# Kernel optimization log

Measured on AMD Instinct MI355X. Metric: run time of the kernel, lower is better.

Reference implementation:

```python
import jax, jax.numpy as jnp
import numpy as np

DIM = 1024
HEADS = 16
HEAD_DIM = DIM // HEADS
NEG = -1e30
EPS = 1e-5


def _linear(x, w, b):
    # torch nn.Linear: y = x @ W^T + b, W: [out, in]
    return jnp.einsum('bnd,od->bno', x, w) + b


def _mha(x, ctx, wq, bq, wk, bk, wv, bv, wo, bo, mask):
    B, N, D = x.shape
    M = ctx.shape[1]
    q = _linear(x, wq, bq).reshape(B, N, HEADS, HEAD_DIM).transpose(0, 2, 1, 3)
    k = _linear(ctx, wk, bk).reshape(B, M, HEADS, HEAD_DIM).transpose(0, 2, 1, 3)
    v = _linear(ctx, wv, bv).reshape(B, M, HEADS, HEAD_DIM).transpose(0, 2, 1, 3)
    scores = jnp.einsum('bhqd,bhkd->bhqk', q, k) / np.sqrt(HEAD_DIM).astype(np.float32)
    if mask is not None:
        scores = jnp.where(mask == 0, NEG, scores)
    attn = jax.nn.softmax(scores, axis=-1)  # dropout = identity (eval mode)
    out = jnp.einsum('bhqk,bhkd->bhqd', attn, v)
    out = out.transpose(0, 2, 1, 3).reshape(B, N, D)
    return _linear(out, wo, bo)


def _ln(x, g, b):
    mu = jnp.mean(x, axis=-1, keepdims=True)
    var = jnp.mean(jnp.square(x - mu), axis=-1, keepdims=True)
    return (x - mu) * jax.lax.rsqrt(var + EPS) * g + b


def setup_inputs() -> dict:
    key = jax.random.key(0)
    ks = jax.random.split(key, 24)
    B, N, M = 2, 2048, 1024
    s = 0.02
    d = {
        'x': jax.random.normal(ks[0], (B, N, DIM), jnp.float32),
        'memory': jax.random.normal(ks[1], (B, M, DIM), jnp.float32),
        'mask': jnp.tril(jnp.ones((N, N), jnp.int32))[None, None],
    }
    i = 2
    for p in ['sa', 'ca']:
        for nm in ['q', 'k', 'v', 'o']:
            d[f'{p}_w{nm}'] = jax.random.normal(ks[i], (DIM, DIM), jnp.float32) * s; i += 1
            d[f'{p}_b{nm}'] = jnp.zeros((DIM,), jnp.float32)
    d['ff_w1'] = jax.random.normal(ks[i], (4 * DIM, DIM), jnp.float32) * s; i += 1
    d['ff_b1'] = jnp.zeros((4 * DIM,), jnp.float32)
    d['ff_w2'] = jax.random.normal(ks[i], (DIM, 4 * DIM), jnp.float32) * s; i += 1
    d['ff_b2'] = jnp.zeros((DIM,), jnp.float32)
    for j in (1, 2, 3):
        d[f'ln{j}_g'] = jnp.ones((DIM,), jnp.float32)
        d[f'ln{j}_b'] = jnp.zeros((DIM,), jnp.float32)
    return d


def reference(x, memory, mask,
              sa_wq, sa_bq, sa_wk, sa_bk, sa_wv, sa_bv, sa_wo, sa_bo,
              ca_wq, ca_bq, ca_wk, ca_bk, ca_wv, ca_bv, ca_wo, ca_bo,
              ff_w1, ff_b1, ff_w2, ff_b2,
              ln1_g, ln1_b, ln2_g, ln2_b, ln3_g, ln3_b):
    x = _ln(x + _mha(x, x, sa_wq, sa_bq, sa_wk, sa_bk, sa_wv, sa_bv, sa_wo, sa_bo, mask), ln1_g, ln1_b)
    x = _ln(x + _mha(x, memory, ca_wq, ca_bq, ca_wk, ca_bk, ca_wv, ca_bv, ca_wo, ca_bo, None), ln2_g, ln2_b)
    h = jax.nn.relu(_linear(x, ff_w1, ff_b1))  # dropout = identity (eval)
    x = _ln(x + _linear(h, ff_w2, ff_b2), ln3_g, ln3_b)
    return x
```

## Files before the change

### kernel.cpp

```cpp
#include <hip/hip_runtime.h>


typedef __attribute__((ext_vector_type(8))) short bf16x8;
typedef __attribute__((ext_vector_type(4))) float f32x4;

__device__ __forceinline__ unsigned short f2bf(float f) {
    union { float f; unsigned int u; } v; v.f = f;
    unsigned int r = v.u + 0x7fffu + ((v.u >> 16) & 1u);
    return (unsigned short)(r >> 16);
}
__device__ __forceinline__ unsigned int bftrunc(float f) {
    union { float f; unsigned int u; } v; v.f = f;
    return v.u >> 16;
}

struct ConvArgs {
    const float* src[12];
    unsigned short* dst[12];
    int blk_ofs[13];
    int n4[12];
};
__global__ __launch_bounds__(256) void conv_multi(ConvArgs a)
{
    int bid = blockIdx.x;
    int s = 0;
#pragma unroll
    for (int t = 0; t < 12; ++t) if (bid >= a.blk_ofs[t + 1]) s = t + 1;
    int i = (bid - a.blk_ofs[s]) * 256 + threadIdx.x;
    if (i >= a.n4[s]) return;
    float4 v = ((const float4*)a.src[s])[i];
    ushort4 o;
    o.x = f2bf(v.x); o.y = f2bf(v.y); o.z = f2bf(v.z); o.w = f2bf(v.w);
    ((ushort4*)a.dst[s])[i] = o;
}

__global__ __launch_bounds__(256) void concat_bias(
    const float* __restrict__ bq, const float* __restrict__ bk,
    const float* __restrict__ bv, const float* __restrict__ ck,
    const float* __restrict__ cv, float* __restrict__ bqkv,
    float* __restrict__ bkvc)
{
    int i = blockIdx.x * 256 + threadIdx.x;
    if (i < 1024)       bqkv[i] = bq[i];
    else if (i < 2048)  bqkv[i] = bk[i - 1024];
    else if (i < 3072)  bqkv[i] = bv[i - 2048];
    else if (i < 4096)  bkvc[i - 3072] = ck[i - 3072];
    else if (i < 5120)  bkvc[i - 3072] = cv[i - 4096];
}

template<int TM, int TN, int EPI, int SK>
__global__ __launch_bounds__(256) void gemm_bt(
    const unsigned short* __restrict__ A, const unsigned short* __restrict__ W,
    const float* __restrict__ bias, void* __restrict__ out,
    int K, int Ncols, long slice_stride)
{
    constexpr int AI = TM / 32;
    constexpr int BJ = TN / 32;
    __shared__ unsigned short As[TM][64];
    __shared__ unsigned short Bs[TN][64];

    const int tid  = threadIdx.x;
    const int lane = tid & 63;
    const int wave = tid >> 6;
    const int qd   = lane >> 4;
    const int l15  = lane & 15;
    const int wm   = (wave >> 1) * (TM / 2);
    const int wn   = (wave & 1) * (TN / 2);

    const int gx  = gridDim.x;
    const int bid = blockIdx.y * gx + blockIdx.x;
    const int gpg = 8 * gx;
    const long m0 = (long)((bid / gpg) * 8 + (bid & 7)) * TM;
    const long n0 = (long)((bid % gpg) >> 3) * TN;

    f32x4 acc[AI][BJ] = {};

    const int srow = lane >> 3;
    const int scol = (((lane & 7) ^ srow)) * 8;
    const unsigned short* Ag = A + (m0 + wave * (8 * AI) + srow) * (long)K + scol;
    const unsigned short* Wg = W + (n0 + wave * (8 * BJ) + srow) * (long)K + scol;

    const int ksl   = K / SK;
    const int kbase = (SK > 1) ? (int)blockIdx.z * ksl : 0;

    for (int k0 = kbase; k0 < kbase + ksl; k0 += 64) {
#pragma unroll
        for (int c = 0; c < AI; ++c)
            __builtin_amdgcn_global_load_lds(
                (const __attribute__((address_space(1))) unsigned int*)(Ag + (long)c * 8 * K + k0),
                (__attribute__((address_space(3))) unsigned int*)((char*)&As[0][0] + (wave * AI + c) * 1024),
                16, 0, 0);
#pragma unroll
        for (int c = 0; c < BJ; ++c)
            __builtin_amdgcn_global_load_lds(
                (const __attribute__((address_space(1))) unsigned int*)(Wg + (long)c * 8 * K + k0),
                (__attribute__((address_space(3))) unsigned int*)((char*)&Bs[0][0] + (wave * BJ + c) * 1024),
                16, 0, 0);
        __syncthreads();
#pragma unroll
        for (int kk = 0; kk < 64; kk += 32) {
            const int pg = ((((kk >> 3) + qd)) ^ (l15 & 7)) * 8;
            bf16x8 af[AI], bw[BJ];
#pragma unroll
            for (int i = 0; i < AI; ++i)
                af[i] = *(const bf16x8*)&As[wm + i * 16 + l15][pg];
#pragma unroll
            for (int j = 0; j < BJ; ++j)
                bw[j] = *(const bf16x8*)&Bs[wn + j * 16 + l15][pg];
#pragma unroll
            for (int i = 0; i < AI; ++i)
#pragma unroll
                for (int j = 0; j < BJ; ++j)
                    acc[i][j] = __builtin_amdgcn_mfma_f32_16x16x32_bf16(
                        af[i], bw[j], acc[i][j], 0, 0, 0);
        }
        __syncthreads();
    }

    float* op = (float*)out + ((SK > 1) ? (long)blockIdx.z * slice_stride : 0);
#pragma unroll
    for (int j = 0; j < BJ; ++j) {
        long col = n0 + wn + j * 16 + l15;
        float bv = (SK == 1 || blockIdx.z == 0) ? bias[col] : 0.f;
#pragma unroll
        for (int i = 0; i < AI; ++i) {
#pragma unroll
            for (int r = 0; r < 4; ++r) {
                long row = m0 + wm + i * 16 + qd * 4 + r;
                float v = acc[i][j][r] + bv;
                if (EPI == 0) {
                    op[row * Ncols + col] = v;
                } else if (EPI == 1) {
                    ((unsigned short*)out)[row * Ncols + col] = f2bf(v);
                } else {
                    ((unsigned short*)out)[row * Ncols + col] = f2bf(v > 0.f ? v : 0.f);
                }
            }
        }
    }
}

__global__ __launch_bounds__(256) void attn_kernel(
    const unsigned short* __restrict__ Qb, int q_stride,
    const unsigned short* __restrict__ KVb, int kv_stride, int koff, int voff,
    unsigned short* __restrict__ O,
    int Nq, int Mk, int causal)
{
    __shared__ unsigned short Ks[64][72];
    __shared__ unsigned short Vs[64][72];
    __shared__ unsigned short Ps[4][16][72];

    const int tid  = threadIdx.x;
    const int lane = tid & 63;
    const int wave = tid >> 6;
    const int qd   = lane >> 4;
    const int l15  = lane & 15;
    const int h    = blockIdx.y;
    const int b    = blockIdx.z;
    int jq = blockIdx.x;
    if (causal && (b & 1)) jq = gridDim.x - 1 - jq;
    const int q0 = jq * 64;
    const int tb = q0 + wave * 16;

    bf16x8 aq0, aq1;
    {
        const unsigned short* qp =
            Qb + (long)(b * Nq + tb + l15) * q_stride + h * 64 + qd * 8;
        aq0 = *(const bf16x8*)qp;
        aq1 = *(const bf16x8*)(qp + 32);
    }

    float lpart[4] = {};
    f32x4 oacc[4] = {};

    const int krow = tid >> 3;
    const int kcol = (tid & 7) * 8;
    const int vj   = tid & 31;
    const int va_k = (vj & 15) + ((vj & 16) << 1);
    const int vfg  = (tid >> 5) * 8;
    const int vpc  = (va_k & 15) * 4 + (va_k >> 4);

    const unsigned short* Kg = KVb + (long)b * Mk * kv_stride + koff + h * 64;
    const unsigned short* Vg = KVb + (long)b * Mk * kv_stride + voff + h * 64;

    bf16x8 kr0, kr1, vra, vrb;
    auto prefetch = [&](int k0) {
        kr0 = *(const bf16x8*)(Kg + (long)(k0 + krow) * kv_stride + kcol);
        kr1 = *(const bf16x8*)(Kg + (long)(k0 + krow + 32) * kv_stride + kcol);
        const unsigned short* v0 = Vg + (long)(k0 + va_k) * kv_stride + vfg;
        vra = *(const bf16x8*)v0;
        vrb = *(const bf16x8*)(v0 + 16 * kv_stride);
    };

    const int nk = causal ? (q0 + 64) : Mk;
    prefetch(0);
    const float SCL = 0.125f * 1.44269504f;

    for (int k0 = 0; k0 < nk; k0 += 64) {
        __syncthreads();
        *(bf16x8*)&Ks[krow][kcol]      = kr0;
        *(bf16x8*)&Ks[krow + 32][kcol] = kr1;
#pragma unroll
        for (int jf = 0; jf < 8; ++jf) {
            unsigned int d = (unsigned short)vra[jf] |
                             ((unsigned int)(unsigned short)vrb[jf] << 16);
            *(unsigned int*)&Vs[vfg + jf][vpc] = d;
        }
        if (k0 + 64 < nk) prefetch(k0 + 64);
        __syncthreads();

        if (!causal || (k0 <= tb + 15)) {
            bf16x8 bk[4][2];
#pragma unroll
            for (int kt = 0; kt < 4; ++kt)
#pragma unroll
                for (int c = 0; c < 2; ++c)
                    bk[kt][c] = *(const bf16x8*)&Ks[kt * 16 + l15][c * 32 + qd * 8];
            f32x4 s[4];
#pragma unroll
            for (int kt = 0; kt < 4; ++kt) {
                f32x4 z = {};
                z = __builtin_amdgcn_mfma_f32_16x16x32_bf16(aq0, bk[kt][0], z, 0, 0, 0);
                z = __builtin_amdgcn_mfma_f32_16x16x32_bf16(aq1, bk[kt][1], z, 0, 0, 0);
                s[kt] = z;
            }
            const bool needmask = causal && (k0 + 63 > tb);
#pragma unroll
            for (int r = 0; r < 4; ++r) {
                const int qg = tb + qd * 4 + r;
                float e[4];
#pragma unroll
                for (int kt = 0; kt < 4; ++kt) {
                    float ev = __builtin_amdgcn_exp2f(s[kt][r] * SCL);
                    if (needmask && (k0 + kt * 16 + l15 > qg)) ev = 0.f;
                    e[kt] = ev;
                }
                lpart[r] += (e[0] + e[1]) + (e[2] + e[3]);
                unsigned int lo = bftrunc(e[0]) | (bftrunc(e[1]) << 16);
                unsigned int hi = bftrunc(e[2]) | (bftrunc(e[3]) << 16);
                uint2 pk; pk.x = lo; pk.y = hi;
                *(uint2*)&Ps[wave][qd * 4 + r][l15 * 4] = pk;
            }
            bf16x8 bv[4][2];
#pragma unroll
            for (int dt = 0; dt < 4; ++dt)
#pragma unroll
                for (int c = 0; c < 2; ++c)
                    bv[dt][c] = *(const bf16x8*)&Vs[dt * 16 + l15][c * 32 + qd * 8];
            bf16x8 ap0 = *(const bf16x8*)&Ps[wave][l15][qd * 8];
            bf16x8 ap1 = *(const bf16x8*)&Ps[wave][l15][32 + qd * 8];
#pragma unroll
            for (int dt = 0; dt < 4; ++dt) {
                oacc[dt] = __builtin_amdgcn_mfma_f32_16x16x32_bf16(
                    ap0, bv[dt][0], oacc[dt], 0, 0, 0);
                oacc[dt] = __builtin_amdgcn_mfma_f32_16x16x32_bf16(
                    ap1, bv[dt][1], oacc[dt], 0, 0, 0);
            }
        }
    }

#pragma unroll
    for (int r = 0; r < 4; ++r) {
        float l = lpart[r];
        l += __shfl_xor(l, 1);
        l += __shfl_xor(l, 2);
        l += __shfl_xor(l, 4);
        l += __shfl_xor(l, 8);
        float inv = 1.f / l;
        long row = (long)(b * Nq + tb + qd * 4 + r);
#pragma unroll
        for (int dt = 0; dt < 4; ++dt)
            O[row * 1024 + h * 64 + dt * 16 + l15] = f2bf(oacc[dt][r] * inv);
    }
}

template<int ND>
__global__ __launch_bounds__(256) void ln_res_kernel(
    const float* __restrict__ res, const float* __restrict__ delta, long dstride,
    const float* __restrict__ g, const float* __restrict__ beta,
    float* __restrict__ yout, unsigned short* __restrict__ ybf)
{
    __shared__ float red[8];
    const int row = blockIdx.x;
    const int tid = threadIdx.x;
    const long base = (long)row * 1024 + tid * 4;
    float4 a = *(const float4*)(res + base);
    float v0 = a.x, v1 = a.y, v2 = a.z, v3 = a.w;
#pragma unroll
    for (int t = 0; t < ND; ++t) {
        float4 d = *(const float4*)(delta + t * dstride + base);
        v0 += d.x; v1 += d.y; v2 += d.z; v3 += d.w;
    }
    float s  = v0 + v1 + v2 + v3;
    float ss = v0 * v0 + v1 * v1 + v2 * v2 + v3 * v3;
#pragma unroll
    for (int off = 1; off < 64; off <<= 1) {
        s  += __shfl_xor(s, off);
        ss += __shfl_xor(ss, off);
    }
    const int wave = tid >> 6;
    if ((tid & 63) == 0) { red[wave] = s; red[4 + wave] = ss; }
    __syncthreads();
    float st  = red[0] + red[1] + red[2] + red[3];
    float sst = red[4] + red[5] + red[6] + red[7];
    float mean = st * (1.f / 1024.f);
    float var  = sst * (1.f / 1024.f) - mean * mean;
    float inv  = rsqrtf(var + 1e-5f);
    const int c = tid * 4;
    float y0 = (v0 - mean) * inv * g[c + 0] + beta[c + 0];
    float y1 = (v1 - mean) * inv * g[c + 1] + beta[c + 1];
    float y2 = (v2 - mean) * inv * g[c + 2] + beta[c + 2];
    float y3 = (v3 - mean) * inv * g[c + 3] + beta[c + 3];
    *(float4*)(yout + base) = make_float4(y0, y1, y2, y3);
    if (ybf) {
        ushort4 o;
        o.x = f2bf(y0); o.y = f2bf(y1); o.z = f2bf(y2); o.w = f2bf(y3);
        *(ushort4*)(ybf + base) = o;
    }
}

extern "C" void kernel_launch(void* const* d_in, const int* in_sizes, int n_in,
                              void* d_out, int out_size, void* d_ws, size_t ws_size,
                              hipStream_t stream)
{
    const int B = 2, N = 2048, M = 1024, D = 1024, FF = 4096;
    const int TN = B * N;
    const int TM = B * M;
    const size_t MB = 1024 * 1024;

    const float* x     = (const float*)d_in[0];
    const float* mem   = (const float*)d_in[1];
    const float* sa_wq = (const float*)d_in[3];  const float* sa_bq = (const float*)d_in[4];
    const float* sa_wk = (const float*)d_in[5];  const float* sa_bk = (const float*)d_in[6];
    const float* sa_wv = (const float*)d_in[7];  const float* sa_bv = (const float*)d_in[8];
    const float* sa_wo = (const float*)d_in[9];  const float* sa_bo = (const float*)d_in[10];
    const float* ca_wq = (const float*)d_in[11]; const float* ca_bq = (const float*)d_in[12];
    const float* ca_wk = (const float*)d_in[13]; const float* ca_bk = (const float*)d_in[14];
    const float* ca_wv = (const float*)d_in[15]; const float* ca_bv = (const float*)d_in[16];
    const float* ca_wo = (const float*)d_in[17]; const float* ca_bo = (const float*)d_in[18];
    const float* ff_w1 = (const float*)d_in[19]; const float* ff_b1 = (const float*)d_in[20];
    const float* ff_w2 = (const float*)d_in[21]; const float* ff_b2 = (const float*)d_in[22];
    const float* ln1_g = (const float*)d_in[23]; const float* ln1_b = (const float*)d_in[24];
    const float* ln2_g = (const float*)d_in[25]; const float* ln2_b = (const float*)d_in[26];
    const float* ln3_g = (const float*)d_in[27]; const float* ln3_b = (const float*)d_in[28];

    char* w = (char*)d_ws;
    size_t off = 0;
    auto alloc = [&](size_t bytes) -> char* {
        char* p = w + off; off += (bytes + 255) & ~(size_t)255; return p;
    };

    unsigned short* xb   = (unsigned short*)alloc((size_t)TN * D * 2);
    unsigned short* memb = (unsigned short*)alloc((size_t)TM * D * 2);
    unsigned short* wqkv = (unsigned short*)alloc((size_t)3 * D * D * 2);
    unsigned short* wos  = (unsigned short*)alloc((size_t)D * D * 2);
    unsigned short* wqc  = (unsigned short*)alloc((size_t)D * D * 2);
    unsigned short* wkvc = (unsigned short*)alloc((size_t)2 * D * D * 2);
    unsigned short* woc  = (unsigned short*)alloc((size_t)D * D * 2);
    unsigned short* w1b  = (unsigned short*)alloc((size_t)FF * D * 2);
    unsigned short* w2b  = (unsigned short*)alloc((size_t)D * FF * 2);
    float* xf = (float*)alloc((size_t)TN * D * 4);
    char* big = alloc((size_t)64 * MB);
    unsigned short* qkv = (unsigned short*)big;
    unsigned short* kvb = (unsigned short*)big;
    unsigned short* qb  = (unsigned short*)(big + 8 * MB);
    unsigned short* ab  = (unsigned short*)(big + 24 * MB);
    unsigned short* hb  = (unsigned short*)big;
    float*          tmp = (float*)(big + 32 * MB);
    const long      TSL = (long)TN * D;
    float* bqkv = (float*)alloc((size_t)3 * D * 4);
    float* bkvc = (float*)alloc((size_t)2 * D * 4);

    ConvArgs ca;
    const float* srcs[12] = {x, mem, sa_wq, sa_wk, sa_wv, sa_wo,
                             ca_wq, ca_wk, ca_wv, ca_wo, ff_w1, ff_w2};
    unsigned short* dsts[12] = {xb, memb, wqkv, wqkv + (size_t)D * D,
                                wqkv + (size_t)2 * D * D, wos, wqc, wkvc,
                                wkvc + (size_t)D * D, woc, w1b, w2b};
    long ns[12] = {(long)TN * D, (long)TM * D, (long)D * D, (long)D * D,
                   (long)D * D, (long)D * D, (long)D * D, (long)D * D,
                   (long)D * D, (long)D * D, (long)FF * D, (long)D * FF};
    int total_blk = 0;
    for (int i = 0; i < 12; ++i) {
        ca.src[i] = srcs[i]; ca.dst[i] = dsts[i];
        ca.n4[i] = (int)(ns[i] / 4);
        ca.blk_ofs[i] = total_blk;
        total_blk += (ca.n4[i] + 255) / 256;
    }
    ca.blk_ofs[12] = total_blk;
    conv_multi<<<dim3(total_blk), dim3(256), 0, stream>>>(ca);
    concat_bias<<<dim3(20), dim3(256), 0, stream>>>(
        sa_bq, sa_bk, sa_bv, ca_bk, ca_bv, bqkv, bkvc);

    dim3 blk(256);

    gemm_bt<128, 128, 1, 1><<<dim3(3 * D / 128, TN / 128), blk, 0, stream>>>(
        xb, wqkv, bqkv, qkv, D, 3 * D, 0);
    attn_kernel<<<dim3(N / 64, 16, B), blk, 0, stream>>>(
        qkv, 3 * D, qkv, 3 * D, D, 2 * D, ab, N, N, 1);
    gemm_bt<128, 64, 0, 2><<<dim3(D / 64, TN / 128, 2), blk, 0, stream>>>(
        ab, wos, sa_bo, tmp, D, D, TSL);
    ln_res_kernel<2><<<dim3(TN), blk, 0, stream>>>(x, tmp, TSL, ln1_g, ln1_b, xf, xb);

    gemm_bt<128, 64, 1, 1><<<dim3(D / 64, TN / 128), blk, 0, stream>>>(
        xb, wqc, ca_bq, qb, D, D, 0);
    gemm_bt<128, 64, 1, 1><<<dim3(2 * D / 64, TM / 128), blk, 0, stream>>>(
        memb, wkvc, bkvc, kvb, D, 2 * D, 0);
    attn_kernel<<<dim3(N / 64, 16, B), blk, 0, stream>>>(
        qb, D, kvb, 2 * D, 0, D, ab, N, M, 0);
    gemm_bt<128, 64, 0, 2><<<dim3(D / 64, TN / 128, 2), blk, 0, stream>>>(
        ab, woc, ca_bo, tmp, D, D, TSL);
    ln_res_kernel<2><<<dim3(TN), blk, 0, stream>>>(xf, tmp, TSL, ln2_g, ln2_b, xf, xb);

    gemm_bt<128, 128, 2, 1><<<dim3(FF / 128, TN / 128), blk, 0, stream>>>(
        xb, w1b, ff_b1, hb, D, FF, 0);
    gemm_bt<128, 64, 0, 2><<<dim3(D / 64, TN / 128, 2), blk, 0, stream>>>(
        hb, w2b, ff_b2, tmp, FF, D, TSL);
    ln_res_kernel<2><<<dim3(TN), blk, 0, stream>>>(xf, tmp, TSL, ln3_g, ln3_b, (float*)d_out, nullptr);
}
```

Measured before the change: 502.0 us.

## Store split-K partials and residual in bf16, fuse cross-attn Q/KV GEMMs

Split-K GEMM partials now go out as bf16 instead of fp32. The residual stream is kept only as bf16, and the fp32 xf buffer is dropped. The cross-attention Q and KV projection GEMMs are merged into one dual launch, and the FFN down-projection uses 4-way split-K with a 4-input LN. This is meant to cut memory traffic and launch count, at the cost of accuracy loss from rounding the residual and the partial sums to bf16.

```diff
diff --git a/kernel.cpp b/kernel.cpp
--- a/kernel.cpp
+++ b/kernel.cpp
@@ -8,6 +8,10 @@
     union { float f; unsigned int u; } v; v.f = f;
     unsigned int r = v.u + 0x7fffu + ((v.u >> 16) & 1u);
     return (unsigned short)(r >> 16);
+}
+__device__ __forceinline__ float bf2f(unsigned short u) {
+    union { unsigned int u; float f; } v; v.u = (unsigned int)u << 16;
+    return v.f;
 }
 __device__ __forceinline__ unsigned int bftrunc(float f) {
     union { float f; unsigned int u; } v; v.f = f;
@@ -49,15 +53,14 @@
 }
 
 template<int TM, int TN, int EPI, int SK>
-__global__ __launch_bounds__(256) void gemm_bt(
+__device__ __forceinline__ void gemm_body(
+    unsigned short (*As)[64], unsigned short (*Bs)[64],
     const unsigned short* __restrict__ A, const unsigned short* __restrict__ W,
-    const float* __restrict__ bias, void* __restrict__ out,
-    int K, int Ncols, long slice_stride)
+    const float* __restrict__ bias, unsigned short* __restrict__ out,
+    int K, int Ncols, long slice_stride, int bid, int gx, int zslice)
 {
     constexpr int AI = TM / 32;
     constexpr int BJ = TN / 32;
-    __shared__ unsigned short As[TM][64];
-    __shared__ unsigned short Bs[TN][64];
 
     const int tid  = threadIdx.x;
     const int lane = tid & 63;
@@ -67,8 +70,6 @@
     const int wm   = (wave >> 1) * (TM / 2);
     const int wn   = (wave & 1) * (TN / 2);
 
-    const int gx  = gridDim.x;
-    const int bid = blockIdx.y * gx + blockIdx.x;
     const int gpg = 8 * gx;
     const long m0 = (long)((bid / gpg) * 8 + (bid & 7)) * TM;
     const long n0 = (long)((bid % gpg) >> 3) * TN;
@@ -81,7 +82,7 @@
     const unsigned short* Wg = W + (n0 + wave * (8 * BJ) + srow) * (long)K + scol;
 
     const int ksl   = K / SK;
-    const int kbase = (SK > 1) ? (int)blockIdx.z * ksl : 0;
+    const int kbase = (SK > 1) ? zslice * ksl : 0;
 
     for (int k0 = kbase; k0 < kbase + ksl; k0 += 64) {
 #pragma unroll
@@ -117,27 +118,51 @@
         __syncthreads();
     }
 
-    float* op = (float*)out + ((SK > 1) ? (long)blockIdx.z * slice_stride : 0);
+    unsigned short* op = out + ((SK > 1) ? (long)zslice * slice_stride : 0);
 #pragma unroll
     for (int j = 0; j < BJ; ++j) {
         long col = n0 + wn + j * 16 + l15;
-        float bv = (SK == 1 || blockIdx.z == 0) ? bias[col] : 0.f;
+        float bv = (SK == 1 || zslice == 0) ? bias[col] : 0.f;
 #pragma unroll
         for (int i = 0; i < AI; ++i) {
 #pragma unroll
             for (int r = 0; r < 4; ++r) {
                 long row = m0 + wm + i * 16 + qd * 4 + r;
                 float v = acc[i][j][r] + bv;
-                if (EPI == 0) {
-                    op[row * Ncols + col] = v;
-                } else if (EPI == 1) {
-                    ((unsigned short*)out)[row * Ncols + col] = f2bf(v);
-                } else {
-                    ((unsigned short*)out)[row * Ncols + col] = f2bf(v > 0.f ? v : 0.f);
-                }
+                if (EPI == 1) v = (v > 0.f) ? v : 0.f;
+                op[row * Ncols + col] = f2bf(v);
             }
         }
     }
+}
+
+template<int TM, int TN, int EPI, int SK>
+__global__ __launch_bounds__(256) void gemm_bt(
+    const unsigned short* __restrict__ A, const unsigned short* __restrict__ W,
+    const float* __restrict__ bias, unsigned short* __restrict__ out,
+    int K, int Ncols, long slice_stride)
+{
+    __shared__ unsigned short As[TM][64];
+    __shared__ unsigned short Bs[TN][64];
+    const int bid = blockIdx.y * gridDim.x + blockIdx.x;
+    gemm_body<TM, TN, EPI, SK>(As, Bs, A, W, bias, out, K, Ncols, slice_stride,
+                               bid, gridDim.x, (int)blockIdx.z);
+}
+
+template<int TM, int TN>
+__global__ __launch_bounds__(256) void gemm_bt_dual(
+    const unsigned short* A0, const unsigned short* W0, const float* b0,
+    unsigned short* o0, int K0, int N0, int gx0, int nb0,
+    const unsigned short* A1, const unsigned short* W1, const float* b1,
+    unsigned short* o1, int K1, int N1, int gx1)
+{
+    __shared__ unsigned short As[TM][64];
+    __shared__ unsigned short Bs[TN][64];
+    const int bid = blockIdx.x;
+    if (bid < nb0)
+        gemm_body<TM, TN, 0, 1>(As, Bs, A0, W0, b0, o0, K0, N0, 0, bid, gx0, 0);
+    else
+        gemm_body<TM, TN, 0, 1>(As, Bs, A1, W1, b1, o1, K1, N1, 0, bid - nb0, gx1, 0);
 }
 
 __global__ __launch_bounds__(256) void attn_kernel(
@@ -274,22 +299,28 @@
     }
 }
 
-template<int ND>
+template<int ND, int RESBF>
 __global__ __launch_bounds__(256) void ln_res_kernel(
-    const float* __restrict__ res, const float* __restrict__ delta, long dstride,
-    const float* __restrict__ g, const float* __restrict__ beta,
+    const void* __restrict__ res, const unsigned short* __restrict__ delta,
+    long dstride, const float* __restrict__ g, const float* __restrict__ beta,
     float* __restrict__ yout, unsigned short* __restrict__ ybf)
 {
     __shared__ float red[8];
     const int row = blockIdx.x;
     const int tid = threadIdx.x;
     const long base = (long)row * 1024 + tid * 4;
-    float4 a = *(const float4*)(res + base);
-    float v0 = a.x, v1 = a.y, v2 = a.z, v3 = a.w;
+    float v0, v1, v2, v3;
+    if (RESBF) {
+        ushort4 a = *(const ushort4*)((const unsigned short*)res + base);
+        v0 = bf2f(a.x); v1 = bf2f(a.y); v2 = bf2f(a.z); v3 = bf2f(a.w);
+    } else {
+        float4 a = *(const float4*)((const float*)res + base);
+        v0 = a.x; v1 = a.y; v2 = a.z; v3 = a.w;
+    }
 #pragma unroll
     for (int t = 0; t < ND; ++t) {
-        float4 d = *(const float4*)(delta + t * dstride + base);
-        v0 += d.x; v1 += d.y; v2 += d.z; v3 += d.w;
+        ushort4 d = *(const ushort4*)(delta + t * dstride + base);
+        v0 += bf2f(d.x); v1 += bf2f(d.y); v2 += bf2f(d.z); v3 += bf2f(d.w);
     }
     float s  = v0 + v1 + v2 + v3;
     float ss = v0 * v0 + v1 * v1 + v2 * v2 + v3 * v3;
@@ -311,7 +342,7 @@
     float y1 = (v1 - mean) * inv * g[c + 1] + beta[c + 1];
     float y2 = (v2 - mean) * inv * g[c + 2] + beta[c + 2];
     float y3 = (v3 - mean) * inv * g[c + 3] + beta[c + 3];
-    *(float4*)(yout + base) = make_float4(y0, y1, y2, y3);
+    if (yout) *(float4*)(yout + base) = make_float4(y0, y1, y2, y3);
     if (ybf) {
         ushort4 o;
         o.x = f2bf(y0); o.y = f2bf(y1); o.z = f2bf(y2); o.w = f2bf(y3);
@@ -359,15 +390,14 @@
     unsigned short* woc  = (unsigned short*)alloc((size_t)D * D * 2);
     unsigned short* w1b  = (unsigned short*)alloc((size_t)FF * D * 2);
     unsigned short* w2b  = (unsigned short*)alloc((size_t)D * FF * 2);
-    float* xf = (float*)alloc((size_t)TN * D * 4);
     char* big = alloc((size_t)64 * MB);
-    unsigned short* qkv = (unsigned short*)big;
-    unsigned short* kvb = (unsigned short*)big;
-    unsigned short* qb  = (unsigned short*)(big + 8 * MB);
-    unsigned short* ab  = (unsigned short*)(big + 24 * MB);
-    unsigned short* hb  = (unsigned short*)big;
-    float*          tmp = (float*)(big + 32 * MB);
-    const long      TSL = (long)TN * D;
+    unsigned short* qkv   = (unsigned short*)big;
+    unsigned short* kvb   = (unsigned short*)big;
+    unsigned short* qb    = (unsigned short*)(big + 8 * MB);
+    unsigned short* ab    = (unsigned short*)(big + 24 * MB);
+    unsigned short* hb    = (unsigned short*)big;
+    unsigned short* tmpbf = (unsigned short*)(big + 32 * MB);
+    const long      TSL   = (long)TN * D;
     float* bqkv = (float*)alloc((size_t)3 * D * 4);
     float* bkvc = (float*)alloc((size_t)2 * D * 4);
 
@@ -394,27 +424,29 @@
 
     dim3 blk(256);
 
-    gemm_bt<128, 128, 1, 1><<<dim3(3 * D / 128, TN / 128), blk, 0, stream>>>(
+    gemm_bt<128, 128, 0, 1><<<dim3(3 * D / 128, TN / 128), blk, 0, stream>>>(
         xb, wqkv, bqkv, qkv, D, 3 * D, 0);
     attn_kernel<<<dim3(N / 64, 16, B), blk, 0, stream>>>(
         qkv, 3 * D, qkv, 3 * D, D, 2 * D, ab, N, N, 1);
     gemm_bt<128, 64, 0, 2><<<dim3(D / 64, TN / 128, 2), blk, 0, stream>>>(
-        ab, wos, sa_bo, tmp, D, D, TSL);
-    ln_res_kernel<2><<<dim3(TN), blk, 0, stream>>>(x, tmp, TSL, ln1_g, ln1_b, xf, xb);
-
-    gemm_bt<128, 64, 1, 1><<<dim3(D / 64, TN / 128), blk, 0, stream>>>(
-        xb, wqc, ca_bq, qb, D, D, 0);
-    gemm_bt<128, 64, 1, 1><<<dim3(2 * D / 64, TM / 128), blk, 0, stream>>>(
-        memb, wkvc, bkvc, kvb, D, 2 * D, 0);
+        ab, wos, sa_bo, tmpbf, D, D, TSL);
+    ln_res_kernel<2, 0><<<dim3(TN), blk, 0, stream>>>(
+        x, tmpbf, TSL, ln1_g, ln1_b, nullptr, xb);
+
+    gemm_bt_dual<128, 64><<<dim3(1024), blk, 0, stream>>>(
+        xb,   wqc,  ca_bq, qb,  D, D,     D / 64,  512,
+        memb, wkvc, bkvc,  kvb, D, 2 * D, 2 * D / 64);
     attn_kernel<<<dim3(N / 64, 16, B), blk, 0, stream>>>(
         qb, D, kvb, 2 * D, 0, D, ab, N, M, 0);
     gemm_bt<128, 64, 0, 2><<<dim3(D / 64, TN / 128, 2), blk, 0, stream>>>(
-        ab, woc, ca_bo, tmp, D, D, TSL);
-    ln_res_kernel<2><<<dim3(TN), blk, 0, stream>>>(xf, tmp, TSL, ln2_g, ln2_b, xf, xb);
-
-    gemm_bt<128, 128, 2, 1><<<dim3(FF / 128, TN / 128), blk, 0, stream>>>(
+        ab, woc, ca_bo, tmpbf, D, D, TSL);
+    ln_res_kernel<2, 1><<<dim3(TN), blk, 0, stream>>>(
+        xb, tmpbf, TSL, ln2_g, ln2_b, nullptr, xb);
+
+    gemm_bt<128, 128, 1, 1><<<dim3(FF / 128, TN / 128), blk, 0, stream>>>(
         xb, w1b, ff_b1, hb, D, FF, 0);
-    gemm_bt<128, 64, 0, 2><<<dim3(D / 64, TN / 128, 2), blk, 0, stream>>>(
-        hb, w2b, ff_b2, tmp, FF, D, TSL);
-    ln_res_kernel<2><<<dim3(TN), blk, 0, stream>>>(xf, tmp, TSL, ln3_g, ln3_b, (float*)d_out, nullptr);
-}
+    gemm_bt<128, 64, 0, 4><<<dim3(D / 64, TN / 128, 4), blk, 0, stream>>>(
+        hb, w2b, ff_b2, tmpbf, FF, D, TSL);
+    ln_res_kernel<4, 1><<<dim3(TN), blk, 0, stream>>>(
+        xb, tmpbf, TSL, ln3_g, ln3_b, (float*)d_out, nullptr);
+}
```

After: 488.6 us. -2.7%, faster.
